# Performance work log

Hardware: AMD Instinct MI355X
Metric: run time of the kernel (lower is better)

The kernel has to match this reference:

```python
import jax, jax.numpy as jnp
import numpy as np

N = 100000
E = 3200000
HID = 256
C = 10
T = 12
D = 8
HEADS = 4
LH = HID // 2  # LSTM hidden = hidden_dim // 2


def setup_inputs() -> dict:
    key = jax.random.key(0)
    ks = jax.random.split(key, 16)
    rn = lambda k, shp, s=0.05: jax.random.normal(k, shp, dtype=jnp.float32) * s
    return {
        "embeddings": jax.random.normal(ks[0], (N, HID), dtype=jnp.float32),
        "predictions": jax.random.normal(ks[1], (N, C), dtype=jnp.float32),
        "temporal_features": jax.random.normal(ks[2], (N, T, D), dtype=jnp.float32),
        "edge_index": jax.random.randint(ks[3], (2, E), 0, N),
        "cW1": rn(ks[4], (HID // 2, HID)), "cb1": jnp.zeros((HID // 2,), jnp.float32),
        "cW2": rn(ks[5], (1, HID // 2)), "cb2": jnp.zeros((1,), jnp.float32),
        "w_ih0": rn(ks[6], (4 * LH, C)), "w_hh0": rn(ks[7], (4 * LH, LH)),
        "b_ih0": jnp.zeros((4 * LH,), jnp.float32), "b_hh0": jnp.zeros((4 * LH,), jnp.float32),
        "w_ih1": rn(ks[8], (4 * LH, LH)), "w_hh1": rn(ks[9], (4 * LH, LH)),
        "b_ih1": jnp.zeros((4 * LH,), jnp.float32), "b_hh1": jnp.zeros((4 * LH,), jnp.float32),
        "gW": rn(ks[10], (C, HEADS * C)), "ga_src": rn(ks[11], (HEADS, C)),
        "ga_dst": rn(ks[12], (HEADS, C)), "gb": jnp.zeros((C,), jnp.float32),
    }


def _lstm_layer(x, w_ih, w_hh, b_ih, b_hh):
    # x: [N, T, I]; PyTorch gate order i, f, g, o
    n = x.shape[0]
    h_dim = w_hh.shape[1]
    def step(carry, xt):
        h, c = carry
        g = xt @ w_ih.T + h @ w_hh.T + b_ih + b_hh  # [N, 4H]
        i, f, gg, o = jnp.split(g, 4, axis=-1)
        c = jax.nn.sigmoid(f) * c + jax.nn.sigmoid(i) * jnp.tanh(gg)
        h = jax.nn.sigmoid(o) * jnp.tanh(c)
        return (h, c), h
    init = (jnp.zeros((n, h_dim), x.dtype), jnp.zeros((n, h_dim), x.dtype))
    _, hs = jax.lax.scan(step, init, jnp.swapaxes(x, 0, 1))  # [T, N, H]
    return jnp.swapaxes(hs, 0, 1)


def _gat(probs, src, dst, gW, ga_src, ga_dst, gb, n):
    x = (probs @ gW).reshape(n, HEADS, C)  # [N, H, C]
    a_s = (x * ga_src).sum(-1)  # [N, H]
    a_d = (x * ga_dst).sum(-1)
    e = jax.nn.leaky_relu(a_s[src] + a_d[dst], 0.2)  # [E, H]
    m = jax.ops.segment_max(e, dst, num_segments=n)
    ex = jnp.exp(e - m[dst])
    s = jax.ops.segment_sum(ex, dst, num_segments=n)
    alpha = ex / (s[dst] + 1e-16)  # edge softmax per destination
    out = jax.ops.segment_sum(alpha[:, :, None] * x[src], dst, num_segments=n)
    return out.mean(axis=1) + gb  # concat=False -> head mean, plus bias


def reference(embeddings, predictions, temporal_features, edge_index,
              cW1, cb1, cW2, cb2,
              w_ih0, w_hh0, b_ih0, b_hh0, w_ih1, w_hh1, b_ih1, b_hh1,
              gW, ga_src, ga_dst, gb):
    n = predictions.shape[0]
    probs = jax.nn.softmax(predictions, axis=-1)
    max_probs = probs.max(axis=-1)
    pseudo_labels = jnp.argmax(probs, axis=-1)

    # confidence_net (dropout inactive in eval)
    h = jax.nn.relu(embeddings @ cW1.T + cb1)
    embedding_confidence = jax.nn.sigmoid(h @ cW2.T + cb2)[:, 0]

    # temporal consistency: same prediction repeated T times through 2-layer LSTM
    t = temporal_features.shape[1]
    pred_seq = jnp.broadcast_to(predictions[:, None, :], (n, t, predictions.shape[1]))
    l1 = _lstm_layer(pred_seq, w_ih0, w_hh0, b_ih0, b_hh0)
    l2 = _lstm_layer(l1, w_ih1, w_hh1, b_ih1, b_hh1)
    temporal_variance = jnp.var(l2, axis=1, ddof=1).mean(axis=-1)  # torch.var unbiased
    temporal_confidence = 1.0 / (1.0 + temporal_variance)

    # self-loops (used by both GATConv and agreement check)
    loops = jnp.arange(n, dtype=edge_index.dtype)
    src = jnp.concatenate([edge_index[0], loops])
    dst = jnp.concatenate([edge_index[1], loops])

    gout = _gat(probs, src, dst, gW, ga_src, ga_dst, gb, n)
    num = (probs * gout).sum(-1)
    den = jnp.maximum(jnp.linalg.norm(probs, axis=-1) * jnp.linalg.norm(gout, axis=-1), 1e-8)
    graph_confidence = ((num / den) + 1.0) / 2.0

    combined = (0.4 * max_probs + 0.2 * embedding_confidence
                + 0.2 * temporal_confidence + 0.2 * graph_confidence)
    confident_mask = combined > 0.85

    # neighborhood agreement via segment-sum scatter (replaces per-edge loop)
    deg = jax.ops.segment_sum(jnp.ones_like(src, jnp.float32), src, num_segments=n)
    oh = jax.nn.one_hot(pseudo_labels, C, dtype=jnp.float32)
    nsum = jax.ops.segment_sum(oh[src], dst, num_segments=n)
    navg = nsum / (deg[:, None] + 1e-8)
    agreement = jnp.take_along_axis(navg, pseudo_labels[:, None], axis=1)[:, 0] >= 0.6
    final_mask = confident_mask & agreement

    entropy = -(probs * jnp.log(probs + 1e-8)).sum(-1)
    uncertainty = entropy / np.log(C).astype(np.float32)

    return (pseudo_labels, combined, final_mask, max_probs,
            embedding_confidence, temporal_confidence, graph_confidence, uncertainty)
```

## Files before the change

kernel.cpp:

```cpp
#include <hip/hip_runtime.h>
#include <hip/hip_bf16.h>


#define HIDN 256
#define NC 10
#define TSTEPS 12
#define NHEADS 4
#define LH 128

typedef __attribute__((ext_vector_type(8))) short short8;
typedef __attribute__((ext_vector_type(4))) float floatx4;

__device__ __forceinline__ unsigned short f2bf(float x) {
  unsigned u = __float_as_uint(x);
  u = u + 0x7FFFu + ((u >> 16) & 1u);
  return (unsigned short)(u >> 16);
}
__device__ __forceinline__ unsigned char f2fp8(float x) {
  return (unsigned char)(__builtin_amdgcn_cvt_pk_fp8_f32(x, 0.f, 0, false) & 0xff);
}
__device__ __forceinline__ float fexp2(float x) { return __builtin_amdgcn_exp2f(x); }
__device__ __forceinline__ float frcpf(float x) { return __builtin_amdgcn_rcpf(x); }
#define LOG2E 1.44269504f
__device__ __forceinline__ float sigf(float x) {
  return frcpf(1.0f + fexp2(-LOG2E * x));
}
__device__ __forceinline__ float sig2(float x) {
  return frcpf(1.f + fexp2(-LOG2E * x));
}
__device__ __forceinline__ float tanh2(float x) {
  return 1.f - 2.f * frcpf(1.f + fexp2((2.f * LOG2E) * x));
}
__device__ __forceinline__ floatx4 mfma16(short8 a, short8 b, floatx4 c) {
  return __builtin_amdgcn_mfma_f32_16x16x32_bf16(a, b, c, 0, 0, 0);
}
__device__ __forceinline__ floatx4 mfma8(long a, long b, floatx4 c) {
  return __builtin_amdgcn_mfma_f32_16x16x32_fp8_fp8(a, b, c, 0, 0, 0);
}

__global__ void pack_kernel(const float* __restrict__ whh0, const float* __restrict__ wih0,
                            const float* __restrict__ wih1, const float* __restrict__ whh1,
                            const float* __restrict__ cw1,
                            unsigned char* __restrict__ PB1,
                            unsigned char* __restrict__ PB2,
                            unsigned short* __restrict__ PBc) {
  int idx = blockIdx.x * 256 + threadIdx.x;
  if (idx < 81920) {
    int j = idx & 7, lane = (idx >> 3) & 63, rest = idx >> 9;
    int g = rest & 3, w = (rest >> 2) & 7, ks = rest >> 5;
    int k = ks * 32 + ((lane >> 4) << 3) + j;
    int u = w * 16 + (lane & 15), row = g * 128 + u;
    float val = 0.f;
    if (k < 128) val = whh0[row * 128 + k];
    else if (k < 138) val = wih0[row * 10 + (k - 128)];
    PB1[idx] = f2fp8(val);
  }
  if (idx < 131072) {
    int j = idx & 7, lane = (idx >> 3) & 63, rest = idx >> 9;
    int g = rest & 3, w = (rest >> 2) & 7, ks = rest >> 5;
    int k = ks * 32 + ((lane >> 4) << 3) + j;
    int u = w * 16 + (lane & 15), row = g * 128 + u;
    float val = (k < 128) ? wih1[row * 128 + k] : whh1[row * 128 + (k - 128)];
    PB2[idx] = f2fp8(val);
  }
  if (idx < 32768) {
    int j = idx & 7, lane = (idx >> 3) & 63, t2 = idx >> 9;
    int ti = t2 & 7, ks = t2 >> 3;
    int n = ti * 16 + (lane & 15);
    int k = ks * 32 + ((lane >> 4) << 3) + j;
    PBc[idx] = f2bf(cw1[n * 256 + k]);
  }
}

__global__ void probs_kernel(const float* __restrict__ pred, const float* __restrict__ gW,
                             const float* __restrict__ gas, const float* __restrict__ gad,
                             float* __restrict__ out,
                             float* __restrict__ wp12,
                             float* __restrict__ was, float* __restrict__ wad,
                             int* __restrict__ wlab, float* __restrict__ wmp, int N) {
  __shared__ float sgW[400], sgas[40], sgad[40];
  int tid = threadIdx.x;
  for (int i = tid; i < 400; i += 256) sgW[i] = gW[i];
  if (tid < 40) { sgas[tid] = gas[tid]; sgad[tid] = gad[tid]; }
  __syncthreads();
  int node = blockIdx.x * 256 + tid;
  if (node >= N) return;
  const float* pr = pred + (size_t)node * NC;
  float p[NC];
#pragma unroll
  for (int c = 0; c < NC; c++) p[c] = pr[c];
  float pm = p[0]; int arg = 0;
#pragma unroll
  for (int c = 1; c < NC; c++) if (p[c] > pm) { pm = p[c]; arg = c; }
  float s = 0.f, prb[NC];
#pragma unroll
  for (int c = 0; c < NC; c++) { prb[c] = __expf(p[c] - pm); s += prb[c]; }
  float inv = 1.f / s;
  float ent = 0.f;
#pragma unroll
  for (int c = 0; c < NC; c++) {
    prb[c] *= inv;
    ent -= prb[c] * __logf(prb[c] + 1e-8f);
  }
  float4* wp = (float4*)(wp12 + (size_t)node * 12);
  wp[0] = make_float4(prb[0], prb[1], prb[2], prb[3]);
  wp[1] = make_float4(prb[4], prb[5], prb[6], prb[7]);
  wp[2] = make_float4(prb[8], prb[9], 0.f, 0.f);
  out[node] = (float)arg;
  out[(size_t)3 * N + node] = inv;
  out[(size_t)7 * N + node] = ent * (1.f / 2.302585093f);
  wlab[node] = arg;
  wmp[node] = inv;
  float xv[40];
#pragma unroll
  for (int hc = 0; hc < 40; hc++) {
    float t = 0.f;
#pragma unroll
    for (int k = 0; k < NC; k++) t += prb[k] * sgW[k * 40 + hc];
    xv[hc] = t;
  }
#pragma unroll
  for (int h = 0; h < NHEADS; h++) {
    float as = 0.f, ad = 0.f;
#pragma unroll
    for (int c = 0; c < NC; c++) { as += xv[h * 10 + c] * sgas[h * 10 + c]; ad += xv[h * 10 + c] * sgad[h * 10 + c]; }
    was[(size_t)node * 4 + h] = as;
    wad[(size_t)node * 4 + h] = ad;
  }
}

__global__ __launch_bounds__(256) void conf_kernel(const float* __restrict__ emb,
                                                   const unsigned short* __restrict__ PBc,
                                                   const float* __restrict__ cb1,
                                                   const float* __restrict__ cw2,
                                                   const float* __restrict__ cb2,
                                                   float* __restrict__ wec, int N) {
  __shared__ __align__(16) unsigned short astage[128 * 264];
  int tid = threadIdx.x;
  int base = blockIdx.x * 128;
  for (int i = tid * 4; i < 128 * 256; i += 1024) {
    int row = i >> 8, col = i & 255;
    float4 v = make_float4(0.f, 0.f, 0.f, 0.f);
    if (base + row < N) v = *(const float4*)(emb + (size_t)(base + row) * 256 + col);
    unsigned short* d = &astage[row * 264 + col];
    d[0] = f2bf(v.x); d[1] = f2bf(v.y); d[2] = f2bf(v.z); d[3] = f2bf(v.w);
  }
  __syncthreads();
  int wave = tid >> 6, lane = tid & 63, quad = lane >> 4, ln = lane & 15;
  float b1f[8], w2f[8];
#pragma unroll
  for (int t = 0; t < 8; t++) { b1f[t] = cb1[t * 16 + ln]; w2f[t] = cw2[t * 16 + ln]; }
  floatx4 acc[2][8];
#pragma unroll
  for (int mi = 0; mi < 2; mi++)
#pragma unroll
    for (int t = 0; t < 8; t++) acc[mi][t] = (floatx4){b1f[t], b1f[t], b1f[t], b1f[t]};
#pragma unroll
  for (int ks = 0; ks < 8; ks++) {
    short8 a0 = *(const short8*)&astage[(wave * 32 + ln) * 264 + ks * 32 + quad * 8];
    short8 a1 = *(const short8*)&astage[(wave * 32 + 16 + ln) * 264 + ks * 32 + quad * 8];
    const unsigned short* bp = PBc + (((size_t)(ks * 8) * 64 + lane) << 3);
#pragma unroll
    for (int t = 0; t < 8; t++) {
      short8 b = *(const short8*)(bp + (size_t)t * 512);
      acc[0][t] = mfma16(a0, b, acc[0][t]);
      acc[1][t] = mfma16(a1, b, acc[1][t]);
    }
  }
  float part[2][4];
#pragma unroll
  for (int mi = 0; mi < 2; mi++)
#pragma unroll
    for (int r = 0; r < 4; r++) {
      float t = 0.f;
#pragma unroll
      for (int ti = 0; ti < 8; ti++) t += fmaxf(acc[mi][ti][r], 0.f) * w2f[ti];
      part[mi][r] = t;
    }
#pragma unroll
  for (int off = 8; off >= 1; off >>= 1)
#pragma unroll
    for (int mi = 0; mi < 2; mi++)
#pragma unroll
      for (int r = 0; r < 4; r++) part[mi][r] += __shfl_xor(part[mi][r], off);
  if (ln == 0) {
    float b2 = cb2[0];
#pragma unroll
    for (int mi = 0; mi < 2; mi++)
#pragma unroll
      for (int r = 0; r < 4; r++) {
        int node = base + wave * 32 + mi * 16 + quad * 4 + r;
        if (node < N) wec[node] = sigf(part[mi][r] + b2);
      }
  }
}

#define HB2 4352

__global__ __launch_bounds__(512, 2) void lstm_kernel(const float* __restrict__ pred,
                                                      const unsigned char* __restrict__ PB1,
                                                      const unsigned char* __restrict__ PB2,
                                                      const float* __restrict__ bih0,
                                                      const float* __restrict__ bhh0,
                                                      const float* __restrict__ bih1,
                                                      const float* __restrict__ bhh1,
                                                      float* __restrict__ wtc, int N) {
  __shared__ __align__(16) unsigned char hb[4 * HB2];
  __shared__ __align__(16) unsigned char xbuf[32 * 40];
  __shared__ float varsum[32];
  int tid = threadIdx.x;
  int base = blockIdx.x * 32;
  for (int i = tid; i < HB2; i += 512) hb[3 * HB2 + i] = 0;
  for (int i = tid; i < 32 * 40; i += 512) {
    int nd = i / 40, o = i - nd * 40;
    float v = 0.f;
    if (o < 10 && base + nd < N) v = pred[(size_t)(base + nd) * NC + o];
    xbuf[i] = f2fp8(v);
  }
  if (tid < 32) varsum[tid] = 0.f;
  int wave = tid >> 6, lane = tid & 63, quad = lane >> 4, ln = lane & 15;
  float b0f[4], b1f[4];
#pragma unroll
  for (int g = 0; g < 4; g++) {
    int row = g * 128 + wave * 16 + ln;
    b0f[g] = bih0[row] + bhh0[row];
    b1f[g] = bih1[row] + bhh1[row];
  }
  long w1r[5][4], w2r[8][4];
#pragma unroll
  for (int ks = 0; ks < 5; ks++)
#pragma unroll
    for (int g = 0; g < 4; g++)
      w1r[ks][g] = *(const long*)(PB1 + (size_t)(((ks * 8 + wave) * 4 + g) * 64 + lane) * 8);
#pragma unroll
  for (int ks = 0; ks < 8; ks++)
#pragma unroll
    for (int g = 0; g < 4; g++)
      w2r[ks][g] = *(const long*)(PB2 + (size_t)(((ks * 8 + wave) * 4 + g) * 64 + lane) * 8);
  float c1[8], c2[8], s1[8], s2[8];
#pragma unroll
  for (int i = 0; i < 8; i++) { c1[i] = 0.f; c2[i] = 0.f; s1[i] = 0.f; s2[i] = 0.f; }
  const int hq = quad * 8;
  const int ucol = wave * 16 + ln;
  int arow[2], wrow[2];
#pragma unroll
  for (int mt = 0; mt < 2; mt++) {
    arow[mt] = (mt * 16 + ln) * 136 + hq;
    wrow[mt] = (mt * 16 + quad * 4) * 136 + ucol;
  }
  __syncthreads();
  long xa[2];
  xa[0] = *(const long*)&xbuf[ln * 40 + hq];
  xa[1] = *(const long*)&xbuf[(16 + ln) * 40 + hq];

  {
    floatx4 acc[2][4];
#pragma unroll
    for (int mt = 0; mt < 2; mt++)
#pragma unroll
      for (int g = 0; g < 4; g++) acc[mt][g] = (floatx4){b0f[g], b0f[g], b0f[g], b0f[g]};
#pragma unroll
    for (int g = 0; g < 4; g++)
#pragma unroll
      for (int mt = 0; mt < 2; mt++) acc[mt][g] = mfma8(xa[mt], w1r[4][g], acc[mt][g]);
#pragma unroll
    for (int mt = 0; mt < 2; mt++)
#pragma unroll
      for (int r = 0; r < 4; r++) {
        int ci = mt * 4 + r;
        float ig = sig2(acc[mt][0][r]);
        float gg = tanh2(acc[mt][2][r]);
        float og = sig2(acc[mt][3][r]);
        float c = ig * gg;
        c1[ci] = c;
        hb[0 + wrow[mt] + r * 136] = f2fp8(og * tanh2(c));
      }
  }

#define LSTM_SEG(O1R, O1W, O2R, O2W, lastseg)                                    \
  {                                                                              \
    __syncthreads();                                                             \
    floatx4 acc[2][4];                                                           \
    _Pragma("unroll") for (int mt = 0; mt < 2; mt++)                             \
        _Pragma("unroll") for (int g = 0; g < 4; g++)                            \
            acc[mt][g] = (floatx4){b1f[g], b1f[g], b1f[g], b1f[g]};              \
    _Pragma("unroll") for (int ks = 0; ks < 8; ks++) {                           \
      long a_[2];                                                                \
      if (ks < 4) {                                                              \
        _Pragma("unroll") for (int mt = 0; mt < 2; mt++)                         \
            a_[mt] = *(const long*)&hb[(O1R) + arow[mt] + ks * 32];              \
      } else {                                                                   \
        _Pragma("unroll") for (int mt = 0; mt < 2; mt++)                         \
            a_[mt] = *(const long*)&hb[(O2R) + arow[mt] + (ks - 4) * 32];        \
      }                                                                          \
      _Pragma("unroll") for (int g = 0; g < 4; g++)                              \
          _Pragma("unroll") for (int mt = 0; mt < 2; mt++)                       \
              acc[mt][g] = mfma8(a_[mt], w2r[ks][g], acc[mt][g]);                \
    }                                                                            \
    _Pragma("unroll") for (int mt = 0; mt < 2; mt++)                             \
        _Pragma("unroll") for (int r = 0; r < 4; r++) {                          \
      int ci = mt * 4 + r;                                                       \
      float ig = sig2(acc[mt][0][r]);                                            \
      float fg = sig2(acc[mt][1][r]);                                            \
      float gg = tanh2(acc[mt][2][r]);                                           \
      float og = sig2(acc[mt][3][r]);                                            \
      float c = fg * c2[ci] + ig * gg;                                           \
      c2[ci] = c;                                                                \
      float h = og * tanh2(c);                                                   \
      s1[ci] += h;                                                               \
      s2[ci] += h * h;                                                           \
      hb[(O2W) + wrow[mt] + r * 136] = f2fp8(h);                                 \
    }                                                                            \
    if (!(lastseg)) {                                                            \
      _Pragma("unroll") for (int mt = 0; mt < 2; mt++)                           \
          _Pragma("unroll") for (int g = 0; g < 4; g++)                          \
              acc[mt][g] = (floatx4){b0f[g], b0f[g], b0f[g], b0f[g]};            \
      _Pragma("unroll") for (int ks = 0; ks < 5; ks++) {                         \
        long a_[2];                                                              \
        if (ks < 4) {                                                            \
          _Pragma("unroll") for (int mt = 0; mt < 2; mt++)                       \
              a_[mt] = *(const long*)&hb[(O1R) + arow[mt] + ks * 32];            \
        } else {                                                                 \
          a_[0] = xa[0]; a_[1] = xa[1];                                          \
        }                                                                        \
        _Pragma("unroll") for (int g = 0; g < 4; g++)                            \
            _Pragma("unroll") for (int mt = 0; mt < 2; mt++)                     \
                acc[mt][g] = mfma8(a_[mt], w1r[ks][g], acc[mt][g]);              \
      }                                                                          \
      _Pragma("unroll") for (int mt = 0; mt < 2; mt++)                           \
          _Pragma("unroll") for (int r = 0; r < 4; r++) {                        \
        int ci = mt * 4 + r;                                                     \
        float ig = sig2(acc[mt][0][r]);                                          \
        float fg = sig2(acc[mt][1][r]);                                          \
        float gg = tanh2(acc[mt][2][r]);                                         \
        float og = sig2(acc[mt][3][r]);                                          \
        float c = fg * c1[ci] + ig * gg;                                         \
        c1[ci] = c;                                                              \
        hb[(O1W) + wrow[mt] + r * 136] = f2fp8(og * tanh2(c));                   \
      }                                                                          \
    }                                                                            \
  }

  for (int tt = 0; tt < TSTEPS / 2; tt++) {
    LSTM_SEG(0, HB2, 3 * HB2, 2 * HB2, false);
    LSTM_SEG(HB2, 0, 2 * HB2, 3 * HB2, tt == TSTEPS / 2 - 1);
  }
#undef LSTM_SEG

#pragma unroll
  for (int mt = 0; mt < 2; mt++)
#pragma unroll
    for (int r = 0; r < 4; r++) {
      int ci = mt * 4 + r;
      float m = s1[ci] * (1.f / 12.f);
      float var = (s2[ci] - 12.f * m * m) * (1.f / 11.f);
      atomicAdd(&varsum[mt * 16 + quad * 4 + r], var);
    }
  __syncthreads();
  if (tid < 32 && base + tid < N)
    wtc[base + tid] = 1.f / (1.f + varsum[tid] * (1.f / 128.f));
}

__global__ void hist_kernel(const int* __restrict__ ei, int* __restrict__ indeg,
                            int* __restrict__ outdeg, int E, int N) {
  int idx = blockIdx.x * 256 + threadIdx.x;
  if (idx >= E + N) return;
  int src, dst;
  if (idx < E) { src = ei[idx]; dst = ei[E + idx]; } else { src = dst = idx - E; }
  atomicAdd(&indeg[dst], 1);
  atomicAdd(&outdeg[src], 1);
}

__global__ void scan1_kernel(const int* __restrict__ indeg, int* __restrict__ rowptr,
                             int* __restrict__ partials, int N) {
  int t = threadIdx.x, b = blockIdx.x;
  int base = b * 1024 + t * 4;
  int v0 = 0, v1 = 0, v2 = 0, v3 = 0;
  if (base + 0 < N) v0 = indeg[base + 0];
  if (base + 1 < N) v1 = indeg[base + 1];
  if (base + 2 < N) v2 = indeg[base + 2];
  if (base + 3 < N) v3 = indeg[base + 3];
  int tsum = v0 + v1 + v2 + v3;
  int lane = t & 63, wv = t >> 6;
  int x = tsum;
#pragma unroll
  for (int d = 1; d < 64; d <<= 1) { int y = __shfl_up(x, d); if (lane >= d) x += y; }
  __shared__ int wsum[4];
  if (lane == 63) wsum[wv] = x;
  __syncthreads();
  int wo = 0;
  for (int i = 0; i < wv; i++) wo += wsum[i];
  int excl = wo + x - tsum;
  if (base + 0 < N) rowptr[base + 0] = excl;
  if (base + 1 < N) rowptr[base + 1] = excl + v0;
  if (base + 2 < N) rowptr[base + 2] = excl + v0 + v1;
  if (base + 3 < N) rowptr[base + 3] = excl + v0 + v1 + v2;
  if (t == 255) partials[b] = wo + x;
}

__global__ void scan2_kernel(int* __restrict__ partials, int nb) {
  int t = threadIdx.x;
  int lane = t & 63, wv = t >> 6;
  int v = (t < nb) ? partials[t] : 0;
  int x = v;
#pragma unroll
  for (int d = 1; d < 64; d <<= 1) { int y = __shfl_up(x, d); if (lane >= d) x += y; }
  __shared__ int wsum[4];
  if (lane == 63) wsum[wv] = x;
  __syncthreads();
  int wo = 0;
  for (int i = 0; i < wv; i++) wo += wsum[i];
  if (t < nb) partials[t] = wo + x - v;
}

__global__ void scan3_kernel(int* __restrict__ rowptr, int* __restrict__ cursor,
                             const int* __restrict__ partials, int N, int total) {
  int i = blockIdx.x * 256 + threadIdx.x;
  if (i < N) {
    int v = rowptr[i] + partials[i >> 10];
    rowptr[i] = v;
    cursor[i] = v;
  }
  if (i == 0) rowptr[N] = total;
}

__global__ void scatter_kernel(const int* __restrict__ ei, int* __restrict__ cursor,
                               int* __restrict__ csr, int E, int N) {
  int idx = blockIdx.x * 256 + threadIdx.x;
  if (idx >= E + N) return;
  int src, dst;
  if (idx < E) { src = ei[idx]; dst = ei[E + idx]; } else { src = dst = idx - E; }
  int pos = atomicAdd(&cursor[dst], 1);
  csr[pos] = src;
}

__global__ __launch_bounds__(256) void gather_final_kernel(
    const int* __restrict__ rowptr, const int* __restrict__ csr,
    const float* __restrict__ was, const float* __restrict__ wad,
    const float* __restrict__ wp12, const int* __restrict__ wlab,
    const int* __restrict__ outdeg, const float* __restrict__ gW,
    const float* __restrict__ gb, const float* __restrict__ wmp,
    const float* __restrict__ wec, const float* __restrict__ wtc,
    float* __restrict__ out, int N) {
  __shared__ float sgW[400];
  for (int i = threadIdx.x; i < 400; i += 256) sgW[i] = gW[i];
  __syncthreads();
  int gid = blockIdx.x * 256 + threadIdx.x;
  int node = gid >> 3, sub = gid & 7, h = sub & 3, par = sub >> 2;
  if (node >= N) return;
  int beg = rowptr[node], end = rowptr[node + 1];
  float ad = wad[(size_t)node * 4 + h];
  int mylab = wlab[node];
  float ssum = 0.f, cnt = 0.f;
  float z[10];
#pragma unroll
  for (int c = 0; c < 10; c++) z[c] = 0.f;
  for (int e = beg + par; e < end; e += 2) {
    int s = csr[e];
    float v = was[(size_t)s * 4 + h] + ad;
    float lr = v >= 0.f ? v : 0.2f * v;
    float ex = fexp2(LOG2E * lr);
    ssum += ex;
    const float4* pp = (const float4*)(wp12 + (size_t)s * 12);
    float4 p0 = pp[0], p1 = pp[1], p2 = pp[2];
    z[0] += ex * p0.x; z[1] += ex * p0.y; z[2] += ex * p0.z; z[3] += ex * p0.w;
    z[4] += ex * p1.x; z[5] += ex * p1.y; z[6] += ex * p1.z; z[7] += ex * p1.w;
    z[8] += ex * p2.x; z[9] += ex * p2.y;
    cnt += (wlab[s] == mylab) ? 1.f : 0.f;
  }
  ssum += __shfl_xor(ssum, 4);
  cnt  += __shfl_xor(cnt, 4);
#pragma unroll
  for (int c = 0; c < 10; c++) z[c] += __shfl_xor(z[c], 4);
  float inv = 1.f / (ssum + 1e-16f);
  float gpart[10];
#pragma unroll
  for (int c = 0; c < 10; c++) {
    float t = 0.f;
#pragma unroll
    for (int k = 0; k < 10; k++) t += z[k] * sgW[k * 40 + h * 10 + c];
    gpart[c] = t * inv;
  }
#pragma unroll
  for (int c = 0; c < 10; c++) {
    gpart[c] += __shfl_xor(gpart[c], 1);
    gpart[c] += __shfl_xor(gpart[c], 2);
  }
  if (sub == 0) {
    float num = 0.f, np2 = 0.f, ng2 = 0.f;
    const float* pn = wp12 + (size_t)node * 12;
#pragma unroll
    for (int c = 0; c < 10; c++) {
      float g = gpart[c] * 0.25f + gb[c];
      float p = pn[c];
      num += p * g;
      np2 += p * p;
      ng2 += g * g;
    }
    float den = fmaxf(sqrtf(np2) * sqrtf(ng2), 1e-8f);
    float gc = (num / den + 1.f) * 0.5f;
    float mp = wmp[node], ec = wec[node], tc = wtc[node];
    float comb = 0.4f * mp + 0.2f * ec + 0.2f * tc + 0.2f * gc;
    float dgv = (float)outdeg[node];
    float navg = cnt / (dgv + 1e-8f);
    bool mask = (comb > 0.85f) && (navg >= 0.6f);
    out[(size_t)1 * N + node] = comb;
    out[(size_t)2 * N + node] = mask ? 1.f : 0.f;
    out[(size_t)4 * N + node] = ec;
    out[(size_t)5 * N + node] = tc;
    out[(size_t)6 * N + node] = gc;
  }
}

extern "C" void kernel_launch(void* const* d_in, const int* in_sizes, int n_in,
                              void* d_out, int out_size, void* d_ws, size_t ws_size,
                              hipStream_t stream) {
  const float* emb  = (const float*)d_in[0];
  const float* pred = (const float*)d_in[1];
  const int*   ei   = (const int*)d_in[3];
  const float* cw1  = (const float*)d_in[4];
  const float* cb1  = (const float*)d_in[5];
  const float* cw2  = (const float*)d_in[6];
  const float* cb2  = (const float*)d_in[7];
  const float* wih0 = (const float*)d_in[8];
  const float* whh0 = (const float*)d_in[9];
  const float* bih0 = (const float*)d_in[10];
  const float* bhh0 = (const float*)d_in[11];
  const float* wih1 = (const float*)d_in[12];
  const float* whh1 = (const float*)d_in[13];
  const float* bih1 = (const float*)d_in[14];
  const float* bhh1 = (const float*)d_in[15];
  const float* gW   = (const float*)d_in[16];
  const float* gas  = (const float*)d_in[17];
  const float* gad  = (const float*)d_in[18];
  const float* gb   = (const float*)d_in[19];

  const int N = in_sizes[0] / HIDN;
  const int E = in_sizes[3] / 2;
  float* out = (float*)d_out;
  float* ws = (float*)d_ws;
  const size_t sN = (size_t)N;

  float* wp12   = ws;
  float* was    = ws + 12 * sN;
  float* wad    = ws + 16 * sN;
  int*   wlab   = (int*)(ws + 20 * sN);
  float* wmp    = ws + 21 * sN;
  float* wec    = ws + 22 * sN;
  float* wtc    = ws + 23 * sN;
  int* indeg    = (int*)(ws + 24 * sN);
  int* outdeg   = (int*)(ws + 25 * sN);
  int* rowptr   = (int*)(ws + 26 * sN);
  int* cursor   = (int*)(ws + 27 * sN) + 64;
  int* csr      = (int*)(ws + 28 * sN) + 128;
  int* partials = (int*)(ws + 29 * sN) + 128 + E;
  float* pbase  = ws + 29 * sN + 128 + E + 256;
  unsigned char* PB1 = (unsigned char*)pbase;
  unsigned char* PB2 = (unsigned char*)(pbase + 20480);
  unsigned short* PBc = (unsigned short*)(pbase + 53248);

  hipMemsetAsync(indeg, 0, 2 * sN * sizeof(int), stream);
  pack_kernel<<<512, 256, 0, stream>>>(whh0, wih0, wih1, whh1, cw1, PB1, PB2, PBc);
  probs_kernel<<<(N + 255) / 256, 256, 0, stream>>>(pred, gW, gas, gad, out, wp12,
                                                    was, wad, wlab, wmp, N);
  conf_kernel<<<(N + 127) / 128, 256, 0, stream>>>(emb, PBc, cb1, cw2, cb2, wec, N);
  lstm_kernel<<<(N + 31) / 32, 512, 0, stream>>>(pred, PB1, PB2, bih0, bhh0, bih1, bhh1,
                                                 wtc, N);
  int ne = E + N;
  hist_kernel<<<(ne + 255) / 256, 256, 0, stream>>>(ei, indeg, outdeg, E, N);
  int nb = (N + 1023) / 1024;
  scan1_kernel<<<nb, 256, 0, stream>>>(indeg, rowptr, partials, N);
  scan2_kernel<<<1, 256, 0, stream>>>(partials, nb);
  scan3_kernel<<<(N + 255) / 256, 256, 0, stream>>>(rowptr, cursor, partials, N, ne);
  scatter_kernel<<<(ne + 255) / 256, 256, 0, stream>>>(ei, cursor, csr, E, N);
  gather_final_kernel<<<(8 * N + 255) / 256, 256, 0, stream>>>(
      rowptr, csr, was, wad, wp12, wlab, outdeg, gW, gb, wmp, wec, wtc, out, N);
}
```

Baseline: 1.568 ms.

## Merge independent kernels into block-partitioned megakernels to overlap LSTM with graph work

Independent stages are combined into shared launches, with block ranges picking the role: probs, weight packing and degree histogram in one; confidence MLP and a single-block serial scan in another; the LSTM interleaved with the GAT gather in a third. A small combine kernel writes the final outputs. The goal is to cut launch count and to let compute-bound LSTM blocks overlap memory-bound gather blocks. The gather now uses 16 threads per node instead of 8, and s_setprio is raised around the MFMA loops. Risks: the one-block serial scan sits behind the conf blocks, and the shared launch bounds (512,4) may increase register pressure on the LSTM path.

```diff
diff --git a/kernel.cpp b/kernel.cpp
--- a/kernel.cpp
+++ b/kernel.cpp
@@ -38,52 +38,18 @@
   return __builtin_amdgcn_mfma_f32_16x16x32_fp8_fp8(a, b, c, 0, 0, 0);
 }
 
-__global__ void pack_kernel(const float* __restrict__ whh0, const float* __restrict__ wih0,
-                            const float* __restrict__ wih1, const float* __restrict__ whh1,
-                            const float* __restrict__ cw1,
-                            unsigned char* __restrict__ PB1,
-                            unsigned char* __restrict__ PB2,
-                            unsigned short* __restrict__ PBc) {
-  int idx = blockIdx.x * 256 + threadIdx.x;
-  if (idx < 81920) {
-    int j = idx & 7, lane = (idx >> 3) & 63, rest = idx >> 9;
-    int g = rest & 3, w = (rest >> 2) & 7, ks = rest >> 5;
-    int k = ks * 32 + ((lane >> 4) << 3) + j;
-    int u = w * 16 + (lane & 15), row = g * 128 + u;
-    float val = 0.f;
-    if (k < 128) val = whh0[row * 128 + k];
-    else if (k < 138) val = wih0[row * 10 + (k - 128)];
-    PB1[idx] = f2fp8(val);
-  }
-  if (idx < 131072) {
-    int j = idx & 7, lane = (idx >> 3) & 63, rest = idx >> 9;
-    int g = rest & 3, w = (rest >> 2) & 7, ks = rest >> 5;
-    int k = ks * 32 + ((lane >> 4) << 3) + j;
-    int u = w * 16 + (lane & 15), row = g * 128 + u;
-    float val = (k < 128) ? wih1[row * 128 + k] : whh1[row * 128 + (k - 128)];
-    PB2[idx] = f2fp8(val);
-  }
-  if (idx < 32768) {
-    int j = idx & 7, lane = (idx >> 3) & 63, t2 = idx >> 9;
-    int ti = t2 & 7, ks = t2 >> 3;
-    int n = ti * 16 + (lane & 15);
-    int k = ks * 32 + ((lane >> 4) << 3) + j;
-    PBc[idx] = f2bf(cw1[n * 256 + k]);
-  }
-}
-
-__global__ void probs_kernel(const float* __restrict__ pred, const float* __restrict__ gW,
-                             const float* __restrict__ gas, const float* __restrict__ gad,
-                             float* __restrict__ out,
-                             float* __restrict__ wp12,
-                             float* __restrict__ was, float* __restrict__ wad,
-                             int* __restrict__ wlab, float* __restrict__ wmp, int N) {
-  __shared__ float sgW[400], sgas[40], sgad[40];
+__device__ __forceinline__ void probs_body(
+    int bb, float* sgW, float* sgas, float* sgad,
+    const float* __restrict__ pred, const float* __restrict__ gW,
+    const float* __restrict__ gas, const float* __restrict__ gad,
+    float* __restrict__ out, float* __restrict__ wp12,
+    float* __restrict__ was, float* __restrict__ wad,
+    int* __restrict__ wlab, float* __restrict__ wmp, int N) {
   int tid = threadIdx.x;
   for (int i = tid; i < 400; i += 256) sgW[i] = gW[i];
   if (tid < 40) { sgas[tid] = gas[tid]; sgad[tid] = gad[tid]; }
   __syncthreads();
-  int node = blockIdx.x * 256 + tid;
+  int node = bb * 256 + tid;
   if (node >= N) return;
   const float* pr = pred + (size_t)node * NC;
   float p[NC];
@@ -129,15 +95,82 @@
   }
 }
 
-__global__ __launch_bounds__(256) void conf_kernel(const float* __restrict__ emb,
-                                                   const unsigned short* __restrict__ PBc,
-                                                   const float* __restrict__ cb1,
-                                                   const float* __restrict__ cw2,
-                                                   const float* __restrict__ cb2,
-                                                   float* __restrict__ wec, int N) {
-  __shared__ __align__(16) unsigned short astage[128 * 264];
+__device__ __forceinline__ void pack_body(
+    int bb, const float* __restrict__ whh0, const float* __restrict__ wih0,
+    const float* __restrict__ wih1, const float* __restrict__ whh1,
+    const float* __restrict__ cw1,
+    unsigned char* __restrict__ PB1, unsigned char* __restrict__ PB2,
+    unsigned short* __restrict__ PBc) {
+  int idx = bb * 256 + threadIdx.x;
+  if (idx < 81920) {
+    int j = idx & 7, lane = (idx >> 3) & 63, rest = idx >> 9;
+    int g = rest & 3, w = (rest >> 2) & 7, ks = rest >> 5;
+    int k = ks * 32 + ((lane >> 4) << 3) + j;
+    int u = w * 16 + (lane & 15), row = g * 128 + u;
+    float val = 0.f;
+    if (k < 128) val = whh0[row * 128 + k];
+    else if (k < 138) val = wih0[row * 10 + (k - 128)];
+    PB1[idx] = f2fp8(val);
+  }
+  if (idx < 131072) {
+    int j = idx & 7, lane = (idx >> 3) & 63, rest = idx >> 9;
+    int g = rest & 3, w = (rest >> 2) & 7, ks = rest >> 5;
+    int k = ks * 32 + ((lane >> 4) << 3) + j;
+    int u = w * 16 + (lane & 15), row = g * 128 + u;
+    float val = (k < 128) ? wih1[row * 128 + k] : whh1[row * 128 + (k - 128)];
+    PB2[idx] = f2fp8(val);
+  }
+  if (idx < 32768) {
+    int j = idx & 7, lane = (idx >> 3) & 63, t2 = idx >> 9;
+    int ti = t2 & 7, ks = t2 >> 3;
+    int n = ti * 16 + (lane & 15);
+    int k = ks * 32 + ((lane >> 4) << 3) + j;
+    PBc[idx] = f2bf(cw1[n * 256 + k]);
+  }
+}
+
+__device__ __forceinline__ void hist_body(
+    int bb, const int* __restrict__ ei, int* __restrict__ indeg,
+    int* __restrict__ outdeg, int E, int N) {
+  int idx = bb * 256 + threadIdx.x;
+  if (idx >= E + N) return;
+  int src, dst;
+  if (idx < E) { src = ei[idx]; dst = ei[E + idx]; } else { src = dst = idx - E; }
+  atomicAdd(&indeg[dst], 1);
+  atomicAdd(&outdeg[src], 1);
+}
+
+__global__ __launch_bounds__(256) void mega1_kernel(
+    const float* __restrict__ pred, const float* __restrict__ gW,
+    const float* __restrict__ gas, const float* __restrict__ gad,
+    float* __restrict__ out, float* __restrict__ wp12,
+    float* __restrict__ was, float* __restrict__ wad,
+    int* __restrict__ wlab, float* __restrict__ wmp,
+    const float* __restrict__ whh0, const float* __restrict__ wih0,
+    const float* __restrict__ wih1, const float* __restrict__ whh1,
+    const float* __restrict__ cw1,
+    unsigned char* __restrict__ PB1, unsigned char* __restrict__ PB2,
+    unsigned short* __restrict__ PBc,
+    const int* __restrict__ ei, int* __restrict__ indeg, int* __restrict__ outdeg,
+    int N, int E, int GP, int GK) {
+  __shared__ float sgW[400], sgas[40], sgad[40];
+  int b = blockIdx.x;
+  if (b < GP) {
+    probs_body(b, sgW, sgas, sgad, pred, gW, gas, gad, out, wp12, was, wad, wlab, wmp, N);
+  } else if (b < GP + GK) {
+    pack_body(b - GP, whh0, wih0, wih1, whh1, cw1, PB1, PB2, PBc);
+  } else {
+    hist_body(b - GP - GK, ei, indeg, outdeg, E, N);
+  }
+}
+
+__device__ __forceinline__ void conf_body(
+    int bb, unsigned short* astage,
+    const float* __restrict__ emb, const unsigned short* __restrict__ PBc,
+    const float* __restrict__ cb1, const float* __restrict__ cw2,
+    const float* __restrict__ cb2, float* __restrict__ wec, int N) {
   int tid = threadIdx.x;
-  int base = blockIdx.x * 128;
+  int base = bb * 128;
   for (int i = tid * 4; i < 128 * 256; i += 1024) {
     int row = i >> 8, col = i & 255;
     float4 v = make_float4(0.f, 0.f, 0.f, 0.f);
@@ -195,22 +228,79 @@
   }
 }
 
+__device__ __forceinline__ void scan_body(
+    int* wsum, const int* __restrict__ indeg, int* __restrict__ rowptr,
+    int* __restrict__ cursor, int N) {
+  int t = threadIdx.x;
+  int lane = t & 63, wv = t >> 6;
+  int runbase = 0;
+  for (int c0 = 0; c0 < N; c0 += 1024) {
+    int i = c0 + t * 4;
+    int v0 = 0, v1 = 0, v2 = 0, v3 = 0;
+    if (i + 0 < N) v0 = indeg[i + 0];
+    if (i + 1 < N) v1 = indeg[i + 1];
+    if (i + 2 < N) v2 = indeg[i + 2];
+    if (i + 3 < N) v3 = indeg[i + 3];
+    int tsum = v0 + v1 + v2 + v3;
+    int x = tsum;
+#pragma unroll
+    for (int d = 1; d < 64; d <<= 1) { int y = __shfl_up(x, d); if (lane >= d) x += y; }
+    if (lane == 63) wsum[wv] = x;
+    __syncthreads();
+    int wo = 0;
+    for (int w = 0; w < wv; w++) wo += wsum[w];
+    int tot = wsum[0] + wsum[1] + wsum[2] + wsum[3];
+    int excl = runbase + wo + x - tsum;
+    if (i + 0 < N) { rowptr[i + 0] = excl; cursor[i + 0] = excl; }
+    if (i + 1 < N) { rowptr[i + 1] = excl + v0; cursor[i + 1] = excl + v0; }
+    if (i + 2 < N) { rowptr[i + 2] = excl + v0 + v1; cursor[i + 2] = excl + v0 + v1; }
+    if (i + 3 < N) { rowptr[i + 3] = excl + v0 + v1 + v2; cursor[i + 3] = excl + v0 + v1 + v2; }
+    runbase += tot;
+    __syncthreads();
+  }
+  if (t == 0) rowptr[N] = runbase;
+}
+
+__global__ __launch_bounds__(256) void mega2_kernel(
+    const float* __restrict__ emb, const unsigned short* __restrict__ PBc,
+    const float* __restrict__ cb1, const float* __restrict__ cw2,
+    const float* __restrict__ cb2, float* __restrict__ wec,
+    const int* __restrict__ indeg, int* __restrict__ rowptr,
+    int* __restrict__ cursor, int N, int GC) {
+  __shared__ __align__(16) unsigned short astage[128 * 264];
+  int b = blockIdx.x;
+  if (b < GC) {
+    conf_body(b, astage, emb, PBc, cb1, cw2, cb2, wec, N);
+  } else {
+    scan_body((int*)astage, indeg, rowptr, cursor, N);
+  }
+}
+
+__global__ void scatter_kernel(const int* __restrict__ ei, int* __restrict__ cursor,
+                               int* __restrict__ csr, int E, int N) {
+  int idx = blockIdx.x * 256 + threadIdx.x;
+  if (idx >= E + N) return;
+  int src, dst;
+  if (idx < E) { src = ei[idx]; dst = ei[E + idx]; } else { src = dst = idx - E; }
+  int pos = atomicAdd(&cursor[dst], 1);
+  csr[pos] = src;
+}
+
 #define HB2 4352
 
-__global__ __launch_bounds__(512, 2) void lstm_kernel(const float* __restrict__ pred,
-                                                      const unsigned char* __restrict__ PB1,
-                                                      const unsigned char* __restrict__ PB2,
-                                                      const float* __restrict__ bih0,
-                                                      const float* __restrict__ bhh0,
-                                                      const float* __restrict__ bih1,
-                                                      const float* __restrict__ bhh1,
-                                                      float* __restrict__ wtc, int N) {
-  __shared__ __align__(16) unsigned char hb[4 * HB2];
-  __shared__ __align__(16) unsigned char xbuf[32 * 40];
-  __shared__ float varsum[32];
+__device__ __forceinline__ void lstm_body(
+    int bL, unsigned char* smem,
+    const float* __restrict__ pred, const unsigned char* __restrict__ PB1,
+    const unsigned char* __restrict__ PB2,
+    const float* __restrict__ bih0, const float* __restrict__ bhh0,
+    const float* __restrict__ bih1, const float* __restrict__ bhh1,
+    float* __restrict__ wtc, int N) {
+  unsigned char* hb = smem;
+  unsigned char* xbuf = smem + 4 * HB2;
+  float* varsum = (float*)(smem + 4 * HB2 + 1280);
   int tid = threadIdx.x;
-  int base = blockIdx.x * 32;
-  for (int i = tid; i < HB2; i += 512) hb[3 * HB2 + i] = 0;
+  int base = bL * 32;
+  for (int i = tid * 4; i < HB2; i += 2048) *(int*)&hb[3 * HB2 + i] = 0;
   for (int i = tid; i < 32 * 40; i += 512) {
     int nd = i / 40, o = i - nd * 40;
     float v = 0.f;
@@ -284,6 +374,7 @@
     _Pragma("unroll") for (int mt = 0; mt < 2; mt++)                             \
         _Pragma("unroll") for (int g = 0; g < 4; g++)                            \
             acc[mt][g] = (floatx4){b1f[g], b1f[g], b1f[g], b1f[g]};              \
+    __builtin_amdgcn_s_setprio(1);                                               \
     _Pragma("unroll") for (int ks = 0; ks < 8; ks++) {                           \
       long a_[2];                                                                \
       if (ks < 4) {                                                              \
@@ -297,6 +388,7 @@
           _Pragma("unroll") for (int mt = 0; mt < 2; mt++)                       \
               acc[mt][g] = mfma8(a_[mt], w2r[ks][g], acc[mt][g]);                \
     }                                                                            \
+    __builtin_amdgcn_s_setprio(0);                                               \
     _Pragma("unroll") for (int mt = 0; mt < 2; mt++)                             \
         _Pragma("unroll") for (int r = 0; r < 4; r++) {                          \
       int ci = mt * 4 + r;                                                       \
@@ -315,6 +407,7 @@
       _Pragma("unroll") for (int mt = 0; mt < 2; mt++)                           \
           _Pragma("unroll") for (int g = 0; g < 4; g++)                          \
               acc[mt][g] = (floatx4){b0f[g], b0f[g], b0f[g], b0f[g]};            \
+      __builtin_amdgcn_s_setprio(1);                                             \
       _Pragma("unroll") for (int ks = 0; ks < 5; ks++) {                         \
         long a_[2];                                                              \
         if (ks < 4) {                                                            \
@@ -327,6 +420,7 @@
             _Pragma("unroll") for (int mt = 0; mt < 2; mt++)                     \
                 acc[mt][g] = mfma8(a_[mt], w1r[ks][g], acc[mt][g]);              \
       }                                                                          \
+      __builtin_amdgcn_s_setprio(0);                                             \
       _Pragma("unroll") for (int mt = 0; mt < 2; mt++)                           \
           _Pragma("unroll") for (int r = 0; r < 4; r++) {                        \
         int ci = mt * 4 + r;                                                     \
@@ -361,92 +455,20 @@
     wtc[base + tid] = 1.f / (1.f + varsum[tid] * (1.f / 128.f));
 }
 
-__global__ void hist_kernel(const int* __restrict__ ei, int* __restrict__ indeg,
-                            int* __restrict__ outdeg, int E, int N) {
-  int idx = blockIdx.x * 256 + threadIdx.x;
-  if (idx >= E + N) return;
-  int src, dst;
-  if (idx < E) { src = ei[idx]; dst = ei[E + idx]; } else { src = dst = idx - E; }
-  atomicAdd(&indeg[dst], 1);
-  atomicAdd(&outdeg[src], 1);
-}
-
-__global__ void scan1_kernel(const int* __restrict__ indeg, int* __restrict__ rowptr,
-                             int* __restrict__ partials, int N) {
-  int t = threadIdx.x, b = blockIdx.x;
-  int base = b * 1024 + t * 4;
-  int v0 = 0, v1 = 0, v2 = 0, v3 = 0;
-  if (base + 0 < N) v0 = indeg[base + 0];
-  if (base + 1 < N) v1 = indeg[base + 1];
-  if (base + 2 < N) v2 = indeg[base + 2];
-  if (base + 3 < N) v3 = indeg[base + 3];
-  int tsum = v0 + v1 + v2 + v3;
-  int lane = t & 63, wv = t >> 6;
-  int x = tsum;
-#pragma unroll
-  for (int d = 1; d < 64; d <<= 1) { int y = __shfl_up(x, d); if (lane >= d) x += y; }
-  __shared__ int wsum[4];
-  if (lane == 63) wsum[wv] = x;
-  __syncthreads();
-  int wo = 0;
-  for (int i = 0; i < wv; i++) wo += wsum[i];
-  int excl = wo + x - tsum;
-  if (base + 0 < N) rowptr[base + 0] = excl;
-  if (base + 1 < N) rowptr[base + 1] = excl + v0;
-  if (base + 2 < N) rowptr[base + 2] = excl + v0 + v1;
-  if (base + 3 < N) rowptr[base + 3] = excl + v0 + v1 + v2;
-  if (t == 255) partials[b] = wo + x;
-}
-
-__global__ void scan2_kernel(int* __restrict__ partials, int nb) {
-  int t = threadIdx.x;
-  int lane = t & 63, wv = t >> 6;
-  int v = (t < nb) ? partials[t] : 0;
-  int x = v;
-#pragma unroll
-  for (int d = 1; d < 64; d <<= 1) { int y = __shfl_up(x, d); if (lane >= d) x += y; }
-  __shared__ int wsum[4];
-  if (lane == 63) wsum[wv] = x;
-  __syncthreads();
-  int wo = 0;
-  for (int i = 0; i < wv; i++) wo += wsum[i];
-  if (t < nb) partials[t] = wo + x - v;
-}
-
-__global__ void scan3_kernel(int* __restrict__ rowptr, int* __restrict__ cursor,
-                             const int* __restrict__ partials, int N, int total) {
-  int i = blockIdx.x * 256 + threadIdx.x;
-  if (i < N) {
-    int v = rowptr[i] + partials[i >> 10];
-    rowptr[i] = v;
-    cursor[i] = v;
-  }
-  if (i == 0) rowptr[N] = total;
-}
-
-__global__ void scatter_kernel(const int* __restrict__ ei, int* __restrict__ cursor,
-                               int* __restrict__ csr, int E, int N) {
-  int idx = blockIdx.x * 256 + threadIdx.x;
-  if (idx >= E + N) return;
-  int src, dst;
-  if (idx < E) { src = ei[idx]; dst = ei[E + idx]; } else { src = dst = idx - E; }
-  int pos = atomicAdd(&cursor[dst], 1);
-  csr[pos] = src;
-}
-
-__global__ __launch_bounds__(256) void gather_final_kernel(
+__device__ __forceinline__ void gather_body(
+    int bg, unsigned char* smem,
     const int* __restrict__ rowptr, const int* __restrict__ csr,
     const float* __restrict__ was, const float* __restrict__ wad,
     const float* __restrict__ wp12, const int* __restrict__ wlab,
     const int* __restrict__ outdeg, const float* __restrict__ gW,
-    const float* __restrict__ gb, const float* __restrict__ wmp,
-    const float* __restrict__ wec, const float* __restrict__ wtc,
-    float* __restrict__ out, int N) {
-  __shared__ float sgW[400];
-  for (int i = threadIdx.x; i < 400; i += 256) sgW[i] = gW[i];
+    const float* __restrict__ gb, float* __restrict__ wgc,
+    float* __restrict__ wag, int N) {
+  float* sgW = (float*)smem;
+  int tid = threadIdx.x;
+  for (int i = tid; i < 400; i += 512) sgW[i] = gW[i];
   __syncthreads();
-  int gid = blockIdx.x * 256 + threadIdx.x;
-  int node = gid >> 3, sub = gid & 7, h = sub & 3, par = sub >> 2;
+  int vgid = bg * 512 + tid;
+  int node = vgid >> 4, sub = vgid & 15, h = sub & 3, par = sub >> 2;
   if (node >= N) return;
   int beg = rowptr[node], end = rowptr[node + 1];
   float ad = wad[(size_t)node * 4 + h];
@@ -455,7 +477,7 @@
   float z[10];
 #pragma unroll
   for (int c = 0; c < 10; c++) z[c] = 0.f;
-  for (int e = beg + par; e < end; e += 2) {
+  for (int e = beg + par; e < end; e += 4) {
     int s = csr[e];
     float v = was[(size_t)s * 4 + h] + ad;
     float lr = v >= 0.f ? v : 0.2f * v;
@@ -468,10 +490,10 @@
     z[8] += ex * p2.x; z[9] += ex * p2.y;
     cnt += (wlab[s] == mylab) ? 1.f : 0.f;
   }
-  ssum += __shfl_xor(ssum, 4);
-  cnt  += __shfl_xor(cnt, 4);
-#pragma unroll
-  for (int c = 0; c < 10; c++) z[c] += __shfl_xor(z[c], 4);
+  ssum += __shfl_xor(ssum, 4); ssum += __shfl_xor(ssum, 8);
+  cnt  += __shfl_xor(cnt, 4);  cnt  += __shfl_xor(cnt, 8);
+#pragma unroll
+  for (int c = 0; c < 10; c++) { z[c] += __shfl_xor(z[c], 4); z[c] += __shfl_xor(z[c], 8); }
   float inv = 1.f / (ssum + 1e-16f);
   float gpart[10];
 #pragma unroll
@@ -498,18 +520,54 @@
       ng2 += g * g;
     }
     float den = fmaxf(sqrtf(np2) * sqrtf(ng2), 1e-8f);
-    float gc = (num / den + 1.f) * 0.5f;
-    float mp = wmp[node], ec = wec[node], tc = wtc[node];
-    float comb = 0.4f * mp + 0.2f * ec + 0.2f * tc + 0.2f * gc;
+    wgc[node] = (num / den + 1.f) * 0.5f;
     float dgv = (float)outdeg[node];
-    float navg = cnt / (dgv + 1e-8f);
-    bool mask = (comb > 0.85f) && (navg >= 0.6f);
-    out[(size_t)1 * N + node] = comb;
-    out[(size_t)2 * N + node] = mask ? 1.f : 0.f;
-    out[(size_t)4 * N + node] = ec;
-    out[(size_t)5 * N + node] = tc;
-    out[(size_t)6 * N + node] = gc;
-  }
+    wag[node] = cnt / (dgv + 1e-8f);
+  }
+}
+
+__global__ __launch_bounds__(512, 4) void mega4_kernel(
+    const float* __restrict__ pred, const unsigned char* __restrict__ PB1,
+    const unsigned char* __restrict__ PB2,
+    const float* __restrict__ bih0, const float* __restrict__ bhh0,
+    const float* __restrict__ bih1, const float* __restrict__ bhh1,
+    float* __restrict__ wtc,
+    const int* __restrict__ rowptr, const int* __restrict__ csr,
+    const float* __restrict__ was, const float* __restrict__ wad,
+    const float* __restrict__ wp12, const int* __restrict__ wlab,
+    const int* __restrict__ outdeg, const float* __restrict__ gW,
+    const float* __restrict__ gb, float* __restrict__ wgc, float* __restrict__ wag,
+    int N, int GL, int GG) {
+  __shared__ __align__(16) unsigned char smem[4 * HB2 + 1280 + 128];
+  int b = blockIdx.x;
+  int mn = GL < GG ? GL : GG, m2 = 2 * mn;
+  int isL, idx;
+  if (b < m2) { isL = !(b & 1); idx = b >> 1; }
+  else { isL = (GL > GG) ? 1 : 0; idx = mn + (b - m2); }
+  if (isL) {
+    lstm_body(idx, smem, pred, PB1, PB2, bih0, bhh0, bih1, bhh1, wtc, N);
+  } else {
+    gather_body(idx, smem, rowptr, csr, was, wad, wp12, wlab, outdeg, gW, gb,
+                wgc, wag, N);
+  }
+}
+
+__global__ void combine_kernel(const float* __restrict__ wmp,
+                               const float* __restrict__ wec,
+                               const float* __restrict__ wtc,
+                               const float* __restrict__ wgc,
+                               const float* __restrict__ wag,
+                               float* __restrict__ out, int N) {
+  int node = blockIdx.x * 256 + threadIdx.x;
+  if (node >= N) return;
+  float mp = wmp[node], ec = wec[node], tc = wtc[node], gc = wgc[node];
+  float comb = 0.4f * mp + 0.2f * ec + 0.2f * tc + 0.2f * gc;
+  bool mask = (comb > 0.85f) && (wag[node] >= 0.6f);
+  out[(size_t)1 * N + node] = comb;
+  out[(size_t)2 * N + node] = mask ? 1.f : 0.f;
+  out[(size_t)4 * N + node] = ec;
+  out[(size_t)5 * N + node] = tc;
+  out[(size_t)6 * N + node] = gc;
 }
 
 extern "C" void kernel_launch(void* const* d_in, const int* in_sizes, int n_in,
@@ -548,31 +606,39 @@
   float* wmp    = ws + 21 * sN;
   float* wec    = ws + 22 * sN;
   float* wtc    = ws + 23 * sN;
-  int* indeg    = (int*)(ws + 24 * sN);
-  int* outdeg   = (int*)(ws + 25 * sN);
-  int* rowptr   = (int*)(ws + 26 * sN);
-  int* cursor   = (int*)(ws + 27 * sN) + 64;
-  int* csr      = (int*)(ws + 28 * sN) + 128;
-  int* partials = (int*)(ws + 29 * sN) + 128 + E;
-  float* pbase  = ws + 29 * sN + 128 + E + 256;
+  float* wgc    = ws + 24 * sN;
+  float* wag    = ws + 25 * sN;
+  int* indeg    = (int*)(ws + 26 * sN);
+  int* outdeg   = (int*)(ws + 27 * sN);
+  int* rowptr   = (int*)(ws + 28 * sN);
+  int* cursor   = (int*)(ws + 29 * sN) + 64;
+  int* csr      = (int*)(ws + 30 * sN) + 128;
+  float* pbase  = ws + 31 * sN + 128 + E;
   unsigned char* PB1 = (unsigned char*)pbase;
   unsigned char* PB2 = (unsigned char*)(pbase + 20480);
   unsigned short* PBc = (unsigned short*)(pbase + 53248);
 
   hipMemsetAsync(indeg, 0, 2 * sN * sizeof(int), stream);
-  pack_kernel<<<512, 256, 0, stream>>>(whh0, wih0, wih1, whh1, cw1, PB1, PB2, PBc);
-  probs_kernel<<<(N + 255) / 256, 256, 0, stream>>>(pred, gW, gas, gad, out, wp12,
-                                                    was, wad, wlab, wmp, N);
-  conf_kernel<<<(N + 127) / 128, 256, 0, stream>>>(emb, PBc, cb1, cw2, cb2, wec, N);
-  lstm_kernel<<<(N + 31) / 32, 512, 0, stream>>>(pred, PB1, PB2, bih0, bhh0, bih1, bhh1,
-                                                 wtc, N);
+
+  int GP = (N + 255) / 256, GK = 512, GH = (E + N + 255) / 256;
+  mega1_kernel<<<GP + GK + GH, 256, 0, stream>>>(
+      pred, gW, gas, gad, out, wp12, was, wad, wlab, wmp,
+      whh0, wih0, wih1, whh1, cw1, PB1, PB2, PBc,
+      ei, indeg, outdeg, N, E, GP, GK);
+
+  int GC = (N + 127) / 128;
+  mega2_kernel<<<GC + 1, 256, 0, stream>>>(
+      emb, PBc, cb1, cw2, cb2, wec, indeg, rowptr, cursor, N, GC);
+
   int ne = E + N;
-  hist_kernel<<<(ne + 255) / 256, 256, 0, stream>>>(ei, indeg, outdeg, E, N);
-  int nb = (N + 1023) / 1024;
-  scan1_kernel<<<nb, 256, 0, stream>>>(indeg, rowptr, partials, N);
-  scan2_kernel<<<1, 256, 0, stream>>>(partials, nb);
-  scan3_kernel<<<(N + 255) / 256, 256, 0, stream>>>(rowptr, cursor, partials, N, ne);
   scatter_kernel<<<(ne + 255) / 256, 256, 0, stream>>>(ei, cursor, csr, E, N);
-  gather_final_kernel<<<(8 * N + 255) / 256, 256, 0, stream>>>(
-      rowptr, csr, was, wad, wp12, wlab, outdeg, gW, gb, wmp, wec, wtc, out, N);
-}
+
+  int GL = (N + 31) / 32;
+  int GG = (16 * N + 511) / 512;
+  mega4_kernel<<<GL + GG, 512, 0, stream>>>(
+      pred, PB1, PB2, bih0, bhh0, bih1, bhh1, wtc,
+      rowptr, csr, was, wad, wp12, wlab, outdeg, gW, gb, wgc, wag,
+      N, GL, GG);
+
+  combine_kernel<<<(N + 255) / 256, 256, 0, stream>>>(wmp, wec, wtc, wgc, wag, out, N);
+}
```

Result: slower. 3.834 ms (+144.4%).
